# Kernel optimization log

Hardware: AMD Instinct MI355X
Metric: run time of the kernel (lower is better)

Reference implementation:

```python
import jax, jax.numpy as jnp
import numpy as np

VOCAB, EMBED, HIDDEN = 32000, 100, 128
B, T = 1024, 256


def setup_inputs() -> dict:
    key = jax.random.key(0)
    ks = jax.random.split(key, 8)
    s_e = 1.0 / np.sqrt(HIDDEN)  # torch nn.RNN init scale
    x = jax.random.randint(ks[0], (B, T), 0, VOCAB, dtype=jnp.int64)
    emb = jax.random.normal(ks[1], (VOCAB, EMBED), dtype=jnp.float32)
    W_ih = jax.random.uniform(ks[2], (HIDDEN, EMBED), jnp.float32, -s_e, s_e)
    W_hh = jax.random.uniform(ks[3], (HIDDEN, HIDDEN), jnp.float32, -s_e, s_e)
    b_ih = jax.random.uniform(ks[4], (HIDDEN,), jnp.float32, -s_e, s_e)
    b_hh = jax.random.uniform(ks[5], (HIDDEN,), jnp.float32, -s_e, s_e)
    s_f = 1.0 / np.sqrt(HIDDEN)
    W_fc = jax.random.uniform(ks[6], (VOCAB, HIDDEN), jnp.float32, -s_f, s_f)
    b_fc = jax.random.uniform(ks[7], (VOCAB,), jnp.float32, -s_f, s_f)
    return {"x": x, "emb": emb, "W_ih": W_ih, "W_hh": W_hh,
            "b_ih": b_ih, "b_hh": b_hh, "W_fc": W_fc, "b_fc": b_fc}


def reference(x, emb, W_ih, W_hh, b_ih, b_hh, W_fc, b_fc):
    # embedding lookup: [B,T] -> [B,T,E]
    embedded = emb[x]
    # precompute input projections for all timesteps: [B,T,H]
    xp = jnp.einsum('bte,he->bth', embedded, W_ih) + b_ih + b_hh
    xp_t = jnp.swapaxes(xp, 0, 1)  # [T,B,H]

    def step(h, xt):
        h = jnp.tanh(xt + h @ W_hh.T)
        return h, None

    h0 = jnp.zeros((x.shape[0], W_hh.shape[0]), dtype=emb.dtype)
    h_last, _ = jax.lax.scan(step, h0, xp_t)
    # final-step linear head: [B,H] -> [B,V]
    return h_last @ W_fc.T + b_fc
```

## Files before the change

kernel.cpp:

```cpp
#include <hip/hip_runtime.h>
#include <hip/hip_bf16.h>

#define V_ 32000
#define E_ 100
#define H_ 128
#define B_ 1024
#define T_ 256

typedef float f32x4 __attribute__((ext_vector_type(4)));
typedef int   i32x4 __attribute__((ext_vector_type(4)));
typedef __bf16 bf16x8 __attribute__((ext_vector_type(8)));
typedef __bf16 bf16x4 __attribute__((ext_vector_type(4)));

__device__ __forceinline__ f32x4 mfma16(bf16x8 a, bf16x8 b, f32x4 c) {
    return __builtin_amdgcn_mfma_f32_16x16x32_bf16(a, b, c, 0, 0, 0);
}

__global__ __launch_bounds__(512, 1) void k0_pp(
    const float* __restrict__ emb, const float* __restrict__ Wih,
    const float* __restrict__ bih, const float* __restrict__ bhh,
    __bf16* __restrict__ pp)
{
    const int tid = threadIdx.x;
    const int lane = tid & 63, w = tid >> 6;
    const int nt = w >> 1;
    const int mh = w & 1;
    const int v0 = blockIdx.x * 64;
    const int sub = lane >> 4, rc = lane & 15;
    const f32x4 z = {0.f, 0.f, 0.f, 0.f};

    bf16x8 af[4][4];
#pragma unroll
    for (int m = 0; m < 4; ++m)
#pragma unroll
        for (int kc = 0; kc < 4; ++kc) {
            int row = (mh * 4 + m) * 16 + rc;
            int k0 = kc * 32 + sub * 8;
            const float* s = Wih + (size_t)row * E_ + k0;
            f32x4 p0 = (k0 + 4 <= E_) ? *(const f32x4*)s : z;
            f32x4 p1 = (k0 + 8 <= E_) ? *(const f32x4*)(s + 4) : z;
            bf16x8 h8;
#pragma unroll
            for (int e = 0; e < 4; ++e) {
                h8[e] = (__bf16)p0[e];
                h8[4 + e] = (__bf16)p1[e];
            }
            af[m][kc] = h8;
        }

    bf16x8 bf[4];
#pragma unroll
    for (int kc = 0; kc < 4; ++kc) {
        int vrow = v0 + nt * 16 + rc;
        int k0 = kc * 32 + sub * 8;
        const float* s = emb + (size_t)vrow * E_ + k0;
        f32x4 p0 = (k0 + 4 <= E_) ? *(const f32x4*)s : z;
        f32x4 p1 = (k0 + 8 <= E_) ? *(const f32x4*)(s + 4) : z;
        bf16x8 h8;
#pragma unroll
        for (int e = 0; e < 4; ++e) {
            h8[e] = (__bf16)p0[e];
            h8[4 + e] = (__bf16)p1[e];
        }
        bf[kc] = h8;
    }

    f32x4 acc[4];
#pragma unroll
    for (int m = 0; m < 4; ++m) {
        int h0 = (mh * 4 + m) * 16 + sub * 4;
        acc[m] = *(const f32x4*)&bih[h0] + *(const f32x4*)&bhh[h0];
    }
#pragma unroll
    for (int kc = 0; kc < 4; ++kc)
#pragma unroll
        for (int m = 0; m < 4; ++m)
            acc[m] = mfma16(af[m][kc], bf[kc], acc[m]);

#pragma unroll
    for (int m = 0; m < 4; ++m) {
        int v = v0 + nt * 16 + rc;
        int h0 = (mh * 4 + m) * 16 + sub * 4;
        bf16x4 o;
#pragma unroll
        for (int r = 0; r < 4; ++r) o[r] = (__bf16)acc[m][r];
        *(bf16x4*)&pp[(size_t)v * H_ + h0] = o;
    }
}

__global__ __launch_bounds__(512, 1) void k2_rnn(
    const int* __restrict__ x, const __bf16* __restrict__ pp,
    const float* __restrict__ Whh, __bf16* __restrict__ hg)
{
    __shared__ __align__(16) __bf16 Hg[2][2048];
    const int tid = threadIdx.x;
    const int lane = tid & 63, w = tid >> 6;
    const int bi = blockIdx.x;
    const int b0 = bi * 16;
    const int sub = lane >> 4, c = lane & 15;

    bf16x8 wah[4];
#pragma unroll
    for (int kc = 0; kc < 4; ++kc) {
        const float* src = Whh + (size_t)(w * 16 + c) * H_ + kc * 32 + sub * 8;
        f32x4 p0 = *(const f32x4*)src, p1 = *(const f32x4*)(src + 4);
        bf16x8 h8;
#pragma unroll
        for (int e = 0; e < 4; ++e) {
            h8[e] = (__bf16)p0[e];
            h8[4 + e] = (__bf16)p1[e];
        }
        wah[kc] = h8;
    }

    if (tid < 256) {
        bf16x8 z8;
#pragma unroll
        for (int e = 0; e < 8; ++e) z8[e] = (__bf16)0.0f;
        *(bf16x8*)&Hg[0][tid * 8] = z8;
    }
    __syncthreads();

    const int i0 = w * 16 + sub * 4;
    const int* xrow = x + (size_t)(b0 + c) * T_;
    const __bf16* ppi = pp + i0;

    const int wb = (((w >> 1) * 64 + ((w & 1) * 2 + (sub >> 1)) * 16 + c) << 3)
                 + (sub & 1) * 4;

    bf16x4 h4;

#define K2_STEP(PK, XREG) do {                                              \
        const __bf16* Hp = &Hg[PK][0];                                      \
        bf16x8 hb0 = *(const bf16x8*)(Hp + lane * 8);                       \
        bf16x8 hb1 = *(const bf16x8*)(Hp + 512 + lane * 8);                 \
        bf16x8 hb2 = *(const bf16x8*)(Hp + 1024 + lane * 8);                \
        bf16x8 hb3 = *(const bf16x8*)(Hp + 1536 + lane * 8);                \
        f32x4 xf;                                                           \
        _Pragma("unroll")                                                   \
        for (int r = 0; r < 4; ++r) xf[r] = (float)XREG[r];                 \
        f32x4 zz = {0.f, 0.f, 0.f, 0.f};                                    \
        f32x4 a0 = mfma16(wah[0], hb0, xf);                                 \
        f32x4 a1 = mfma16(wah[1], hb1, zz);                                 \
        a0 = mfma16(wah[2], hb2, a0);                                       \
        a1 = mfma16(wah[3], hb3, a1);                                       \
        f32x4 s = a0 + a1;                                                  \
        _Pragma("unroll")                                                   \
        for (int r = 0; r < 4; ++r) {                                       \
            float e;                                                        \
            asm("v_exp_f32 %0, %1" : "=v"(e) : "v"(s[r] * 2.8853900817779268f)); \
            float ep1 = e + 1.0f;                                           \
            float rcp;                                                      \
            asm("v_rcp_f32 %0, %1" : "=v"(rcp) : "v"(ep1));                 \
            h4[r] = (__bf16)(1.0f - 2.0f * rcp);                            \
        }                                                                   \
        *(bf16x4*)&Hg[(PK) ^ 1][wb] = h4;                                   \
        asm volatile("s_waitcnt lgkmcnt(0)" ::: "memory");                  \
        __builtin_amdgcn_s_barrier();                                       \
        __builtin_amdgcn_sched_barrier(0);                                  \
    } while (0)

    i32x4 xsA = *(const i32x4*)(xrow);
    bf16x4 xc0 = *(const bf16x4*)(ppi + (size_t)xsA[0] * H_);
    bf16x4 xc1 = *(const bf16x4*)(ppi + (size_t)xsA[1] * H_);
    bf16x4 xc2 = *(const bf16x4*)(ppi + (size_t)xsA[2] * H_);
    bf16x4 xc3 = *(const bf16x4*)(ppi + (size_t)xsA[3] * H_);
    xsA = *(const i32x4*)(xrow + 4);

    for (int j = 0; j < T_ / 4; ++j) {
        bf16x4 xn0, xn1, xn2, xn3;
        i32x4 xsB = xsA;
        if (j < T_ / 4 - 1) {
            xn0 = *(const bf16x4*)(ppi + (size_t)xsA[0] * H_);
            xn1 = *(const bf16x4*)(ppi + (size_t)xsA[1] * H_);
            xn2 = *(const bf16x4*)(ppi + (size_t)xsA[2] * H_);
            xn3 = *(const bf16x4*)(ppi + (size_t)xsA[3] * H_);
        }
        if (j < T_ / 4 - 2)
            xsB = *(const i32x4*)(xrow + 4 * (j + 2));
        K2_STEP(0, xc0);
        K2_STEP(1, xc1);
        K2_STEP(0, xc2);
        K2_STEP(1, xc3);
        xc0 = xn0; xc1 = xn1; xc2 = xn2; xc3 = xn3;
        xsA = xsB;
    }
#undef K2_STEP

    *(bf16x4*)&hg[(size_t)(bi >> 3) * 16384 + (size_t)(bi & 7) * 2048 + wb] = h4;
}

__global__ __launch_bounds__(512, 1) void k3_head(
    const float* __restrict__ Wfc, const __bf16* __restrict__ hg,
    const float* __restrict__ bfc, float* __restrict__ out)
{
    const int tid = threadIdx.x;
    const int lane = tid & 63, w = tid >> 6;
    const int gv = blockIdx.x;
    const int v0 = gv * 128;
    const int sub = lane >> 4, rc = lane & 15;
    const int mt0 = (w & 3) * 2, nt0 = (w >> 2) * 4;

    bf16x8 af[2][4];
#pragma unroll
    for (int m = 0; m < 2; ++m)
#pragma unroll
        for (int kc = 0; kc < 4; ++kc) {
            int row = v0 + (mt0 + m) * 16 + rc;
            const float* src = Wfc + (size_t)row * H_ + (kc * 4 + sub) * 8;
            f32x4 p0 = *(const f32x4*)src, p1 = *(const f32x4*)(src + 4);
            bf16x8 h8;
#pragma unroll
            for (int e = 0; e < 4; ++e) {
                h8[e] = (__bf16)p0[e];
                h8[4 + e] = (__bf16)p1[e];
            }
            af[m][kc] = h8;
        }

    f32x4 bias4[2];
#pragma unroll
    for (int m = 0; m < 2; ++m)
        bias4[m] = *(const f32x4*)&bfc[v0 + (mt0 + m) * 16 + sub * 4];

    for (int bt = 0; bt < 8; ++bt) {
        const int b0 = bt * 128;
        f32x4 acc[2][4];
#pragma unroll
        for (int m = 0; m < 2; ++m)
#pragma unroll
            for (int n = 0; n < 4; ++n) acc[m][n] = (f32x4){0.f, 0.f, 0.f, 0.f};

#pragma unroll
        for (int kc = 0; kc < 4; ++kc) {
            bf16x8 bf[4];
#pragma unroll
            for (int n = 0; n < 4; ++n)
                bf[n] = *(const bf16x8*)&hg[(size_t)bt * 16384
                          + (size_t)(((nt0 + n) * 256) + kc * 64 + lane) * 8];
#pragma unroll
            for (int n = 0; n < 4; ++n)
#pragma unroll
                for (int m = 0; m < 2; ++m)
                    acc[m][n] = mfma16(af[m][kc], bf[n], acc[m][n]);
        }
#pragma unroll
        for (int n = 0; n < 4; ++n)
#pragma unroll
            for (int m = 0; m < 2; ++m) {
                f32x4 v = acc[m][n] + bias4[m];
                float* dst = out + (size_t)(b0 + (nt0 + n) * 16 + rc) * V_
                                 + v0 + (mt0 + m) * 16 + sub * 4;
                *(f32x4*)dst = v;
            }
    }
}

extern "C" void kernel_launch(void* const* d_in, const int* in_sizes, int n_in,
                              void* d_out, int out_size, void* d_ws, size_t ws_size,
                              hipStream_t stream) {
    const int*   x   = (const int*)d_in[0];
    const float* emb = (const float*)d_in[1];
    const float* Wih = (const float*)d_in[2];
    const float* Whh = (const float*)d_in[3];
    const float* bih = (const float*)d_in[4];
    const float* bhh = (const float*)d_in[5];
    const float* Wfc = (const float*)d_in[6];
    const float* bfc = (const float*)d_in[7];
    float* out = (float*)d_out;

    const size_t SZ_HG = 262144;
    const size_t SZ_PP = (size_t)V_ * H_ * 2;

    char* wsb = (char*)d_ws;
    size_t off = 0;
    auto take = [&](size_t n) -> char* {
        char* p = wsb + off;
        off += (n + 255) & ~(size_t)255;
        return p;
    };
    auto fits = [&](size_t n) { return off + n + 256 <= ws_size; };

    __bf16* hgp = (__bf16*)take(SZ_HG);
    __bf16* pp = fits(SZ_PP) ? (__bf16*)take(SZ_PP) : (__bf16*)d_out;

    k0_pp<<<dim3(500), 512, 0, stream>>>(emb, Wih, bih, bhh, pp);
    k2_rnn<<<dim3(64), 512, 0, stream>>>(x, pp, Whh, hgp);
    k3_head<<<dim3(250), 512, 0, stream>>>(Wfc, hgp, bfc, out);
}
```

Measured before the change: 151.7 us.

## Pre-gather projected embeddings into time-major buffer before RNN kernel

Adds a gather kernel that materializes the per-token input projections into a contiguous [T,B,H] bf16 buffer, so the serial RNN kernel reads linear rows instead of doing dependent index loads followed by random gathers from the projection table. This takes the dependent index-then-gather latency off the recurrence's critical path. In exchange it writes and reads an extra 64 MB buffer and adds a kernel launch, and the buffer may spill into the output allocation if the workspace is too small.

```diff
diff --git a/kernel.cpp b/kernel.cpp
--- a/kernel.cpp
+++ b/kernel.cpp
@@ -88,9 +88,23 @@
     }
 }
 
+__global__ __launch_bounds__(256, 4) void k1_gather(
+    const int* __restrict__ x, const __bf16* __restrict__ pp,
+    __bf16* __restrict__ xpb)
+{
+    size_t i = (size_t)blockIdx.x * 256 + threadIdx.x;
+    size_t row = i >> 4;
+    int k8 = (int)(i & 15) * 8;
+    int t = (int)(row >> 10);
+    int b = (int)(row & 1023);
+    int idx = x[(size_t)b * T_ + t];
+    bf16x8 v = *(const bf16x8*)&pp[(size_t)idx * H_ + k8];
+    *(bf16x8*)&xpb[row * H_ + k8] = v;
+}
+
 __global__ __launch_bounds__(512, 1) void k2_rnn(
-    const int* __restrict__ x, const __bf16* __restrict__ pp,
-    const float* __restrict__ Whh, __bf16* __restrict__ hg)
+    const __bf16* __restrict__ xpb, const float* __restrict__ Whh,
+    __bf16* __restrict__ hg)
 {
     __shared__ __align__(16) __bf16 Hg[2][2048];
     const int tid = threadIdx.x;
@@ -122,8 +136,8 @@
     __syncthreads();
 
     const int i0 = w * 16 + sub * 4;
-    const int* xrow = x + (size_t)(b0 + c) * T_;
-    const __bf16* ppi = pp + i0;
+    const __bf16* xq = xpb + (size_t)(b0 + c) * H_ + i0;
+    const size_t xstep = (size_t)B_ * H_;
 
     const int wb = (((w >> 1) * 64 + ((w & 1) * 2 + (sub >> 1)) * 16 + c) << 3)
                  + (sub & 1) * 4;
@@ -160,30 +174,26 @@
         __builtin_amdgcn_sched_barrier(0);                                  \
     } while (0)
 
-    i32x4 xsA = *(const i32x4*)(xrow);
-    bf16x4 xc0 = *(const bf16x4*)(ppi + (size_t)xsA[0] * H_);
-    bf16x4 xc1 = *(const bf16x4*)(ppi + (size_t)xsA[1] * H_);
-    bf16x4 xc2 = *(const bf16x4*)(ppi + (size_t)xsA[2] * H_);
-    bf16x4 xc3 = *(const bf16x4*)(ppi + (size_t)xsA[3] * H_);
-    xsA = *(const i32x4*)(xrow + 4);
+    bf16x4 xc0 = *(const bf16x4*)(xq);
+    bf16x4 xc1 = *(const bf16x4*)(xq + xstep);
+    bf16x4 xc2 = *(const bf16x4*)(xq + 2 * xstep);
+    bf16x4 xc3 = *(const bf16x4*)(xq + 3 * xstep);
+    xq += 4 * xstep;
 
     for (int j = 0; j < T_ / 4; ++j) {
         bf16x4 xn0, xn1, xn2, xn3;
-        i32x4 xsB = xsA;
         if (j < T_ / 4 - 1) {
-            xn0 = *(const bf16x4*)(ppi + (size_t)xsA[0] * H_);
-            xn1 = *(const bf16x4*)(ppi + (size_t)xsA[1] * H_);
-            xn2 = *(const bf16x4*)(ppi + (size_t)xsA[2] * H_);
-            xn3 = *(const bf16x4*)(ppi + (size_t)xsA[3] * H_);
-        }
-        if (j < T_ / 4 - 2)
-            xsB = *(const i32x4*)(xrow + 4 * (j + 2));
+            xn0 = *(const bf16x4*)(xq);
+            xn1 = *(const bf16x4*)(xq + xstep);
+            xn2 = *(const bf16x4*)(xq + 2 * xstep);
+            xn3 = *(const bf16x4*)(xq + 3 * xstep);
+            xq += 4 * xstep;
+        }
         K2_STEP(0, xc0);
         K2_STEP(1, xc1);
         K2_STEP(0, xc2);
         K2_STEP(1, xc3);
         xc0 = xn0; xc1 = xn1; xc2 = xn2; xc3 = xn3;
-        xsA = xsB;
     }
 #undef K2_STEP
 
@@ -269,8 +279,9 @@
     const float* bfc = (const float*)d_in[7];
     float* out = (float*)d_out;
 
-    const size_t SZ_HG = 262144;
-    const size_t SZ_PP = (size_t)V_ * H_ * 2;
+    const size_t SZ_HG  = 262144;
+    const size_t SZ_PP  = (size_t)V_ * H_ * 2;
+    const size_t SZ_XPB = (size_t)T_ * B_ * H_ * 2;
 
     char* wsb = (char*)d_ws;
     size_t off = 0;
@@ -279,12 +290,21 @@
         off += (n + 255) & ~(size_t)255;
         return p;
     };
+    char* outb = (char*)d_out;
+    size_t ooff = 0;
+    auto takeOut = [&](size_t n) -> char* {
+        char* p = outb + ooff;
+        ooff += (n + 255) & ~(size_t)255;
+        return p;
+    };
     auto fits = [&](size_t n) { return off + n + 256 <= ws_size; };
 
     __bf16* hgp = (__bf16*)take(SZ_HG);
-    __bf16* pp = fits(SZ_PP) ? (__bf16*)take(SZ_PP) : (__bf16*)d_out;
+    __bf16* pp  = fits(SZ_PP)  ? (__bf16*)take(SZ_PP)  : (__bf16*)takeOut(SZ_PP);
+    __bf16* xpb = fits(SZ_XPB) ? (__bf16*)take(SZ_XPB) : (__bf16*)takeOut(SZ_XPB);
 
     k0_pp<<<dim3(500), 512, 0, stream>>>(emb, Wih, bih, bhh, pp);
-    k2_rnn<<<dim3(64), 512, 0, stream>>>(x, pp, Whh, hgp);
+    k1_gather<<<dim3(16384), 256, 0, stream>>>(x, pp, xpb);
+    k2_rnn<<<dim3(64), 512, 0, stream>>>(xpb, Whh, hgp);
     k3_head<<<dim3(250), 512, 0, stream>>>(Wfc, hgp, bfc, out);
 }
```

New measurement: 152.5 us (median of 2 runs). About the same (+0.5%).
